# Kernel tuning notes

Hardware: AMD Instinct MI355X
Metric: run time of the kernel (lower is better)

## Reference

```python
import jax, jax.numpy as jnp
import numpy as np

B, N, H = 2, 2048, 1024
NUM_HEADS, HEAD_DIM = 16, 64
SCALE = HEAD_DIM ** -0.5


def setup_inputs() -> dict:
    key = jax.random.key(0)
    ks = jax.random.split(key, 9)
    hidden_states = jax.random.normal(ks[0], (B, N, H), dtype=jnp.float32)
    # ancestor-only mask: lower-triangular incl. diagonal (chain tree)
    tree_mask = jnp.tril(jnp.ones((N, N), dtype=jnp.int32))
    s = H ** -0.5
    Wq = jax.random.normal(ks[1], (H, NUM_HEADS * HEAD_DIM), dtype=jnp.float32) * s
    Wk = jax.random.normal(ks[2], (H, NUM_HEADS * HEAD_DIM), dtype=jnp.float32) * s
    Wv = jax.random.normal(ks[3], (H, NUM_HEADS * HEAD_DIM), dtype=jnp.float32) * s
    Wo = jax.random.normal(ks[4], (NUM_HEADS * HEAD_DIM, H), dtype=jnp.float32) * s
    bq = jnp.zeros((NUM_HEADS * HEAD_DIM,), dtype=jnp.float32)
    bk = jnp.zeros((NUM_HEADS * HEAD_DIM,), dtype=jnp.float32)
    bv = jnp.zeros((NUM_HEADS * HEAD_DIM,), dtype=jnp.float32)
    bo = jnp.zeros((H,), dtype=jnp.float32)
    return {"hidden_states": hidden_states, "tree_mask": tree_mask,
            "Wq": Wq, "bq": bq, "Wk": Wk, "bk": bk,
            "Wv": Wv, "bv": bv, "Wo": Wo, "bo": bo}


def reference(hidden_states, tree_mask, Wq, bq, Wk, bk, Wv, bv, Wo, bo):
    b, n, _ = hidden_states.shape
    q = (hidden_states @ Wq + bq).reshape(b, n, NUM_HEADS, HEAD_DIM)
    k = (hidden_states @ Wk + bk).reshape(b, n, NUM_HEADS, HEAD_DIM)
    v = (hidden_states @ Wv + bv).reshape(b, n, NUM_HEADS, HEAD_DIM)
    # scores: [b, heads, n, n]
    scores = jnp.einsum('bqhd,bkhd->bhqk', q, k) * SCALE
    neg_inf = jnp.finfo(scores.dtype).min
    scores = jnp.where(tree_mask[None, None, :, :] == 0, neg_inf, scores)
    attn = jax.nn.softmax(scores, axis=-1)  # dropout p=0.0 -> identity
    out = jnp.einsum('bhqk,bkhd->bqhd', attn, v).reshape(b, n, NUM_HEADS * HEAD_DIM)
    return out @ Wo + bo
```

## Files before the change

kernel.cpp:

```cpp
#include <hip/hip_runtime.h>
#include <hip/hip_bf16.h>
#include <stdint.h>

typedef unsigned short u16;
typedef short short8 __attribute__((ext_vector_type(8)));
typedef float f32x4 __attribute__((ext_vector_type(4)));
typedef u16 u16x4 __attribute__((ext_vector_type(4)));

#define SCLOG 0.18033688011112042f

static __device__ __forceinline__ u16 f2bf(float f) {
  unsigned u = __float_as_uint(f);
  unsigned rnd = 0x7fffu + ((u >> 16) & 1u);
  return (u16)((u + rnd) >> 16);
}

static __device__ __forceinline__ unsigned pk_bf16(float a, float b) {
  unsigned r;
  asm("v_cvt_pk_bf16_f32 %0, %1, %2" : "=v"(r) : "v"(a), "v"(b));
  return r;
}

static __device__ __forceinline__ void gload_lds16(const void* g, void* l) {
  __builtin_amdgcn_global_load_lds(
      (const __attribute__((address_space(1))) unsigned int*)g,
      (__attribute__((address_space(3))) unsigned int*)l, 16, 0, 0);
}

__global__ __launch_bounds__(256) void prep_kernel(
    const float* __restrict__ hs, const int* __restrict__ mask,
    const float* __restrict__ Wq, const float* __restrict__ Wk,
    const float* __restrict__ Wv, const float* __restrict__ Wo,
    u16* __restrict__ X, u16* __restrict__ WT,
    unsigned long long* __restrict__ bits) {
  __shared__ float tile[32][33];
  const int bid = blockIdx.x;
  const int tid = threadIdx.x;
  if (bid < 4096) {
    const int i = bid * 256 + tid;
    const float4 v = reinterpret_cast<const float4*>(hs)[i];
    u16x4 o;
    o[0] = f2bf(v.x); o[1] = f2bf(v.y); o[2] = f2bf(v.z); o[3] = f2bf(v.w);
    reinterpret_cast<u16x4*>(X)[i] = o;
  } else if (bid < 8192) {
    const int B = bid - 4096;
    const int z = B >> 10, y = (B >> 5) & 31, x = B & 31;
    const float* src = (z == 0) ? Wq : (z == 1) ? Wk : (z == 2) ? Wv : Wo;
    u16* dst = WT + (size_t)z * 1024 * 1024;
    const int row0 = y * 32, col0 = x * 32;
    const int tx = tid & 31, ty = tid >> 5;
#pragma unroll
    for (int i = 0; i < 4; ++i)
      tile[ty + i * 8][tx] = src[(size_t)(row0 + ty + i * 8) * 1024 + col0 + tx];
    __syncthreads();
#pragma unroll
    for (int i = 0; i < 4; ++i) {
      const int r = ty + i * 8;
      dst[(size_t)(col0 + r) * 1024 + row0 + tx] = f2bf(tile[tx][r]);
    }
  } else {
    const int gw = (bid - 8192) * 4 + (tid >> 6);
    const int lane = tid & 63;
    const int q = gw >> 5, w = gw & 31;
    const int mv = mask[(size_t)q * 2048 + w * 64 + lane];
    const unsigned long long bal = __ballot(mv != 0);
    if (lane == 0) bits[(size_t)q * 32 + w] = bal;
  }
}

__global__ __launch_bounds__(256) void gemm_qkv_kernel(
    const u16* __restrict__ X, const u16* __restrict__ WT,
    const float* __restrict__ bq, const float* __restrict__ bk, const float* __restrict__ bv,
    u16* __restrict__ Qb, u16* __restrict__ Kb, u16* __restrict__ Vb) {
  __shared__ u16 As[128 * 32];
  __shared__ u16 Bs[128 * 32];
  const int tid = threadIdx.x;
  const int lane = tid & 63, wid = tid >> 6;
  const int l15 = lane & 15, lg = lane >> 4;
  const int wg = blockIdx.x;
  const int xcd = wg & 7, idx = wg >> 3;
  const int n0 = (xcd * 3 + (idx >> 5)) * 128;
  const int m0 = (idx & 31) * 128;
  const int wr = wid >> 1, wc = wid & 1;

  f32x4 acc[4][4] = {};

  for (int kt = 0; kt < 32; ++kt) {
    __syncthreads();
#pragma unroll
    for (int p = 0; p < 2; ++p) {
      const int c = p * 256 + tid;
      const int r = c >> 2, ch = c & 3;
      gload_lds16(X + (size_t)(m0 + r) * 1024 + kt * 32 + ch * 8,
                  &As[(p * 256 + wid * 64) * 8]);
      gload_lds16(WT + (size_t)(n0 + r) * 1024 + kt * 32 + ch * 8,
                  &Bs[(p * 256 + wid * 64) * 8]);
    }
    __syncthreads();
    short8 af[4], bfr[4];
#pragma unroll
    for (int i = 0; i < 4; ++i) {
      af[i] = *reinterpret_cast<const short8*>(&As[(wr * 64 + i * 16 + l15) * 32 + lg * 8]);
      bfr[i] = *reinterpret_cast<const short8*>(&Bs[(wc * 64 + i * 16 + l15) * 32 + lg * 8]);
    }
#pragma unroll
    for (int i = 0; i < 4; ++i)
#pragma unroll
      for (int j = 0; j < 4; ++j)
        acc[i][j] = __builtin_amdgcn_mfma_f32_16x16x32_bf16(bfr[j], af[i], acc[i][j], 0, 0, 0);
  }

#pragma unroll
  for (int i = 0; i < 4; ++i) {
    const int m = m0 + wr * 64 + i * 16 + l15;
    const int bb = m >> 11, t = m & 2047;
#pragma unroll
    for (int j = 0; j < 4; ++j) {
      const int n = n0 + wc * 64 + j * 16 + lg * 4;
      const float* bsrc = (n < 1024) ? (bq + n) : (n < 2048) ? (bk + n - 1024) : (bv + n - 2048);
      const float4 b4 = *reinterpret_cast<const float4*>(bsrc);
      const float scl = (n < 1024) ? SCLOG : 1.0f;
      u16* dst = (n < 1024) ? Qb : (n < 2048) ? Kb : Vb;
      const int nl = n & 1023;
      const int hh = nl >> 6, d0 = nl & 63;
      uint2 pk;
      pk.x = pk_bf16((acc[i][j][0] + b4.x) * scl, (acc[i][j][1] + b4.y) * scl);
      pk.y = pk_bf16((acc[i][j][2] + b4.z) * scl, (acc[i][j][3] + b4.w) * scl);
      *reinterpret_cast<uint2*>(dst + ((size_t)(bb * 16 + hh) * 2048 + t) * 64 + d0) = pk;
    }
  }
}

__global__ __launch_bounds__(256) void transpose_v_kernel(const u16* __restrict__ Vb,
                                                          u16* __restrict__ VT) {
  __shared__ u16 tile[64][68];
  const int tid = threadIdx.x;
  const int tt = blockIdx.x & 31;
  const int bh = blockIdx.x >> 5;
  const size_t base = (size_t)bh * 2048 * 64;
  const int t0 = tt * 64;
#pragma unroll
  for (int p = 0; p < 2; ++p) {
    int i = p * 256 + tid;
    int row = i >> 3, ch = i & 7;
    *reinterpret_cast<short8*>(&tile[row][ch * 8]) =
        *reinterpret_cast<const short8*>(Vb + base + (size_t)(t0 + row) * 64 + ch * 8);
  }
  __syncthreads();
#pragma unroll
  for (int p = 0; p < 2; ++p) {
    int i = p * 256 + tid;
    int d = i >> 3, ch = i & 7;
    short8 v;
#pragma unroll
    for (int j = 0; j < 8; ++j) v[j] = tile[ch * 8 + j][d];
    *reinterpret_cast<short8*>(VT + base + (size_t)d * 2048 + t0 + ch * 8) = v;
  }
}

struct AttnState {
  f32x4 O[4];
  float l;
  short8 qf0, qf1;
};

static __device__ __forceinline__ void attn_tile(
    AttnState& st, const u16* __restrict__ Kb_, const u16* __restrict__ Vb_,
    u16* __restrict__ pwave, unsigned long long w,
    int l15, int lg, int slg) {
  f32x4 sT[4] = {};
  __builtin_amdgcn_s_setprio(1);
#pragma unroll
  for (int dc = 0; dc < 2; ++dc) {
    const short8 qv = dc ? st.qf1 : st.qf0;
#pragma unroll
    for (int sub = 0; sub < 4; ++sub) {
      const short8 kf = *reinterpret_cast<const short8*>(
          &Kb_[dc * 2048 + (sub * 16 + l15) * 32 + slg]);
      sT[sub] = __builtin_amdgcn_mfma_f32_16x16x32_bf16(kf, qv, sT[sub], 0, 0, 0);
    }
  }
  __builtin_amdgcn_s_setprio(0);

  if (!__all(w == ~0ull)) {
    const unsigned mlo = (unsigned)w, mhi = (unsigned)(w >> 32);
#pragma unroll
    for (int sub = 0; sub < 4; ++sub) {
      const unsigned f = ((sub & 2) ? mhi : mlo) >> ((sub & 1) * 16 + lg * 4);
#pragma unroll
      for (int r = 0; r < 4; ++r)
        sT[sub][r] = ((f >> r) & 1u) ? sT[sub][r] : -1e30f;
    }
  }

  float lsum = 0.f;
#pragma unroll
  for (int kc = 0; kc < 2; ++kc) {
#pragma unroll
    for (int s2 = 0; s2 < 2; ++s2) {
      const int sub = kc * 2 + s2;
      const float e0 = exp2f(sT[sub][0]);
      const float e1 = exp2f(sT[sub][1]);
      const float e2 = exp2f(sT[sub][2]);
      const float e3 = exp2f(sT[sub][3]);
      lsum += (e0 + e1) + (e2 + e3);
      uint2 pk;
      pk.x = pk_bf16(e0, e1);
      pk.y = pk_bf16(e2, e3);
      *reinterpret_cast<uint2*>(&pwave[l15 * 40 + s2 * 16 + lg * 4]) = pk;
    }
    const short8 pf = *reinterpret_cast<const short8*>(&pwave[l15 * 40 + lg * 8]);
    __builtin_amdgcn_s_setprio(1);
#pragma unroll
    for (int dt = 0; dt < 4; ++dt) {
      const short8 vf = *reinterpret_cast<const short8*>(
          &Vb_[kc * 2048 + (dt * 16 + l15) * 32 + slg]);
      st.O[dt] = __builtin_amdgcn_mfma_f32_16x16x32_bf16(vf, pf, st.O[dt], 0, 0, 0);
    }
    __builtin_amdgcn_s_setprio(0);
  }
  st.l += lsum;
}

__global__ __launch_bounds__(256, 4) void attn_kernel(
    const u16* __restrict__ Q, const u16* __restrict__ K, const u16* __restrict__ VT,
    const unsigned long long* __restrict__ MB, u16* __restrict__ AO) {
  __shared__ u16 K_lds[2][4096];
  __shared__ u16 V_lds[2][4096];
  __shared__ u16 p_lds[4][16][40];
  __shared__ unsigned actA_s, actB_s;

  const int tid = threadIdx.x;
  const int wid = tid >> 6, lane = tid & 63;
  const int l15 = lane & 15, lg = lane >> 4;

  const int wgid = blockIdx.x;
  const int x = wgid & 7, s = wgid >> 3;
  const int g = x + 8 * (s >> 5);
  const int qp = s & 31;
  const int h = g & 15, b = g >> 4;
  const int qA_t = qp, qB_t = 63 - qp;
  const size_t bh_off = ((size_t)(b * 16 + h)) * 2048 * 64;

  if (tid == 0) { actA_s = 0; actB_s = 0; }
  __syncthreads();
  {
    const int ktc = tid & 31, rg = tid >> 5;
    unsigned long long orA = 0, orB = 0;
#pragma unroll
    for (int i = 0; i < 4; ++i) {
      orA |= MB[(size_t)(qA_t * 32 + rg * 4 + i) * 32 + ktc];
      orB |= MB[(size_t)(qB_t * 32 + rg * 4 + i) * 32 + ktc];
    }
    if (orA) atomicOr(&actA_s, 1u << ktc);
    if (orB) atomicOr(&actB_s, 1u << ktc);
  }

  const int sid = wid >> 1;
  const int qt = sid ? qB_t : qA_t;
  const int q = qt * 32 + (wid & 1) * 16 + l15;

  AttnState st;
  {
    const short8* qp_ = reinterpret_cast<const short8*>(Q + bh_off + (size_t)q * 64);
    st.qf0 = qp_[lg]; st.qf1 = qp_[4 + lg];
#pragma unroll
    for (int dt = 0; dt < 4; ++dt) st.O[dt] = f32x4{};
    st.l = 0.f;
  }

  const int slg = (lg ^ ((l15 >> 1) & 3)) * 8;

  int offK[2], offV[2], ldsi[2];
#pragma unroll
  for (int p = 0; p < 2; ++p) {
    const int i = wid * 128 + p * 64 + lane;
    const int pc = i >> 8, row = (i >> 2) & 63, lgc = i & 3;
    const int lgs = lgc ^ ((i >> 3) & 3);
    offK[p] = row * 64 + pc * 32 + lgs * 8;
    offV[p] = row * 2048 + pc * 32 + lgs * 8;
    ldsi[p] = (wid * 128 + p * 64) * 8;
  }
  const u16* Kg = K + bh_off;
  const u16* Vg = VT + bh_off;
  u16* pwave = &p_lds[wid][0][0];

  __syncthreads();
  const unsigned actA = actA_s, actB = actB_s;
  const unsigned actW = sid ? actB : actA;
  unsigned rem = actA | actB;
  int buf = 0;

#define STAGE_TILE(bb, ktv)                                        \
  do {                                                             \
    const u16* ksrc_ = Kg + (ktv) * 64 * 64;                       \
    const u16* vsrc_ = Vg + (ktv) * 64;                            \
    _Pragma("unroll") for (int p_ = 0; p_ < 2; ++p_) {             \
      gload_lds16(ksrc_ + offK[p_], &K_lds[bb][ldsi[p_]]);         \
      gload_lds16(vsrc_ + offV[p_], &V_lds[bb][ldsi[p_]]);         \
    }                                                              \
  } while (0)

  if (rem) {
    int kt = __ffs(rem) - 1;
    unsigned long long w_cur = MB[(size_t)q * 32 + kt];
    STAGE_TILE(0, kt);
    __syncthreads();

    while (true) {
      rem &= rem - 1;
      int ktn = -1;
      unsigned long long w_next = 0;
      if (rem) {
        ktn = __ffs(rem) - 1;
        w_next = MB[(size_t)q * 32 + ktn];
        STAGE_TILE(buf ^ 1, ktn);
      }

      if ((actW >> kt) & 1u)
        attn_tile(st, &K_lds[buf][0], &V_lds[buf][0], pwave, w_cur, l15, lg, slg);

      if (ktn < 0) break;
      __syncthreads();
      buf ^= 1;
      kt = ktn;
      w_cur = w_next;
    }
  }
#undef STAGE_TILE

  {
    float lr = st.l;
    lr += __shfl_xor(lr, 16);
    lr += __shfl_xor(lr, 32);
    const float inv = (lr > 0.f) ? (1.0f / lr) : 0.f;
    u16* dst = AO + ((size_t)(b * 2048 + q)) * 1024 + h * 64;
#pragma unroll
    for (int dt = 0; dt < 4; ++dt) {
      uint2 pk;
      pk.x = pk_bf16(st.O[dt][0] * inv, st.O[dt][1] * inv);
      pk.y = pk_bf16(st.O[dt][2] * inv, st.O[dt][3] * inv);
      *reinterpret_cast<uint2*>(dst + dt * 16 + lg * 4) = pk;
    }
  }
}

__global__ __launch_bounds__(256) void gemm_out_kernel(
    const u16* __restrict__ A, const u16* __restrict__ BT,
    const float* __restrict__ bo, float* __restrict__ out) {
  __shared__ u16 As[128 * 32];
  __shared__ u16 Bs[128 * 32];
  const int tid = threadIdx.x;
  const int lane = tid & 63, wid = tid >> 6;
  const int l15 = lane & 15, lg = lane >> 4;
  const int wg = blockIdx.x;
  const int n0 = (wg & 7) * 128;
  const int m0 = (wg >> 3) * 128;
  const int wr = wid >> 1, wc = wid & 1;

  f32x4 acc[4][4] = {};

  for (int kt = 0; kt < 32; ++kt) {
    __syncthreads();
#pragma unroll
    for (int p = 0; p < 2; ++p) {
      const int c = p * 256 + tid;
      const int r = c >> 2, ch = c & 3;
      gload_lds16(A + (size_t)(m0 + r) * 1024 + kt * 32 + ch * 8,
                  &As[(p * 256 + wid * 64) * 8]);
      gload_lds16(BT + (size_t)(n0 + r) * 1024 + kt * 32 + ch * 8,
                  &Bs[(p * 256 + wid * 64) * 8]);
    }
    __syncthreads();
    short8 af[4], bfr[4];
#pragma unroll
    for (int i = 0; i < 4; ++i) {
      af[i] = *reinterpret_cast<const short8*>(&As[(wr * 64 + i * 16 + l15) * 32 + lg * 8]);
      bfr[i] = *reinterpret_cast<const short8*>(&Bs[(wc * 64 + i * 16 + l15) * 32 + lg * 8]);
    }
#pragma unroll
    for (int i = 0; i < 4; ++i)
#pragma unroll
      for (int j = 0; j < 4; ++j)
        acc[i][j] = __builtin_amdgcn_mfma_f32_16x16x32_bf16(bfr[j], af[i], acc[i][j], 0, 0, 0);
  }

#pragma unroll
  for (int i = 0; i < 4; ++i) {
    const int m = m0 + wr * 64 + i * 16 + l15;
#pragma unroll
    for (int j = 0; j < 4; ++j) {
      const int n = n0 + wc * 64 + j * 16 + lg * 4;
      const float4 b4 = *reinterpret_cast<const float4*>(bo + n);
      float4 o4;
      o4.x = acc[i][j][0] + b4.x;
      o4.y = acc[i][j][1] + b4.y;
      o4.z = acc[i][j][2] + b4.z;
      o4.w = acc[i][j][3] + b4.w;
      *reinterpret_cast<float4*>(out + (size_t)m * 1024 + n) = o4;
    }
  }
}

extern "C" void kernel_launch(void* const* d_in, const int* in_sizes, int n_in,
                              void* d_out, int out_size, void* d_ws, size_t ws_size,
                              hipStream_t stream) {
  (void)in_sizes; (void)n_in; (void)out_size; (void)ws_size;
  const float* hs = (const float*)d_in[0];
  const int* mask = (const int*)d_in[1];
  const float* Wq = (const float*)d_in[2];
  const float* bq = (const float*)d_in[3];
  const float* Wk = (const float*)d_in[4];
  const float* bk = (const float*)d_in[5];
  const float* Wv = (const float*)d_in[6];
  const float* bv = (const float*)d_in[7];
  const float* Wo = (const float*)d_in[8];
  const float* bo = (const float*)d_in[9];
  float* out = (float*)d_out;

  uint8_t* ws = (uint8_t*)d_ws;
  u16* X  = (u16*)(ws);
  u16* WT = (u16*)(ws + ((size_t)8 << 20));
  u16* Qb = (u16*)(ws + ((size_t)16 << 20));
  u16* Kb = (u16*)(ws + ((size_t)24 << 20));
  u16* Vb = (u16*)(ws + ((size_t)32 << 20));
  u16* AO = (u16*)(ws + ((size_t)40 << 20));
  unsigned long long* MB = (unsigned long long*)(ws + ((size_t)48 << 20));
  u16* VbT = X;

  prep_kernel<<<dim3(24576), dim3(256), 0, stream>>>(hs, mask, Wq, Wk, Wv, Wo, X, WT, MB);
  gemm_qkv_kernel<<<dim3(768), dim3(256), 0, stream>>>(X, WT, bq, bk, bv, Qb, Kb, Vb);
  transpose_v_kernel<<<dim3(1024), dim3(256), 0, stream>>>(Vb, VbT);
  attn_kernel<<<dim3(1024), dim3(256), 0, stream>>>(Qb, Kb, VbT, MB, AO);
  gemm_out_kernel<<<dim3(256), dim3(256), 0, stream>>>(AO, WT + (size_t)3072 * 1024, bo, out);
}
```

Measured before the change: 133.7 us.

## Rewrite attention with 32x32 MFMA, per-wave query tiles, and permlane P reshuffle

The attention kernel switches from 16x16x32 to 32x32x16 bf16 MFMAs, so each wave owns a full 32-query tile and four waves share one block's K/V staging. That halves the grid to 512 blocks with balanced causal pairs (p, 31-p, 32+p, 63-p). The P matrix is moved between lanes with v_permlane32_swap instead of a round trip through LDS, and the K/V LDS layout uses a new XOR swizzle. Active tiles are found with a ballot instead of shared atomics. Register pressure rises (launch bounds drop to 2 waves/SIMD) and occupancy falls, in exchange for more K/V reuse per block and fewer LDS operations.

```diff
diff --git a/kernel.cpp b/kernel.cpp
--- a/kernel.cpp
+++ b/kernel.cpp
@@ -5,9 +5,12 @@
 typedef unsigned short u16;
 typedef short short8 __attribute__((ext_vector_type(8)));
 typedef float f32x4 __attribute__((ext_vector_type(4)));
+typedef float f32x16 __attribute__((ext_vector_type(16)));
 typedef u16 u16x4 __attribute__((ext_vector_type(4)));
+typedef unsigned uint32x4 __attribute__((ext_vector_type(4)));
 
 #define SCLOG 0.18033688011112042f
+#define MFMA32(A, B, C) __builtin_amdgcn_mfma_f32_32x32x16_bf16(A, B, C, 0, 0, 0)
 
 static __device__ __forceinline__ u16 f2bf(float f) {
   unsigned u = __float_as_uint(f);
@@ -158,142 +161,127 @@
   }
 }
 
-struct AttnState {
-  f32x4 O[4];
-  float l;
-  short8 qf0, qf1;
-};
-
-static __device__ __forceinline__ void attn_tile(
-    AttnState& st, const u16* __restrict__ Kb_, const u16* __restrict__ Vb_,
-    u16* __restrict__ pwave, unsigned long long w,
-    int l15, int lg, int slg) {
-  f32x4 sT[4] = {};
+static __device__ __forceinline__ void attn_tile32(
+    f32x16& O0, f32x16& O1, float& lacc, const short8 qf[4],
+    const u16* __restrict__ Kb_, const u16* __restrict__ Vb_,
+    unsigned long long w, int l31, int hi) {
+  f32x16 s0 = {}, s1 = {};
+  const int r7 = l31 & 7;
   __builtin_amdgcn_s_setprio(1);
 #pragma unroll
-  for (int dc = 0; dc < 2; ++dc) {
-    const short8 qv = dc ? st.qf1 : st.qf0;
-#pragma unroll
-    for (int sub = 0; sub < 4; ++sub) {
-      const short8 kf = *reinterpret_cast<const short8*>(
-          &Kb_[dc * 2048 + (sub * 16 + l15) * 32 + slg]);
-      sT[sub] = __builtin_amdgcn_mfma_f32_16x16x32_bf16(kf, qv, sT[sub], 0, 0, 0);
-    }
+  for (int dc = 0; dc < 4; ++dc) {
+    const int sl = (dc * 2 + hi) ^ r7;
+    const short8 kf0 = *reinterpret_cast<const short8*>(&Kb_[l31 * 64 + sl * 8]);
+    const short8 kf1 = *reinterpret_cast<const short8*>(&Kb_[(32 + l31) * 64 + sl * 8]);
+    s0 = MFMA32(kf0, qf[dc], s0);
+    s1 = MFMA32(kf1, qf[dc], s1);
   }
   __builtin_amdgcn_s_setprio(0);
 
-  if (!__all(w == ~0ull)) {
-    const unsigned mlo = (unsigned)w, mhi = (unsigned)(w >> 32);
-#pragma unroll
-    for (int sub = 0; sub < 4; ++sub) {
-      const unsigned f = ((sub & 2) ? mhi : mlo) >> ((sub & 1) * 16 + lg * 4);
-#pragma unroll
-      for (int r = 0; r < 4; ++r)
-        sT[sub][r] = ((f >> r) & 1u) ? sT[sub][r] : -1e30f;
-    }
-  }
-
-  float lsum = 0.f;
-#pragma unroll
-  for (int kc = 0; kc < 2; ++kc) {
-#pragma unroll
-    for (int s2 = 0; s2 < 2; ++s2) {
-      const int sub = kc * 2 + s2;
-      const float e0 = exp2f(sT[sub][0]);
-      const float e1 = exp2f(sT[sub][1]);
-      const float e2 = exp2f(sT[sub][2]);
-      const float e3 = exp2f(sT[sub][3]);
-      lsum += (e0 + e1) + (e2 + e3);
-      uint2 pk;
-      pk.x = pk_bf16(e0, e1);
-      pk.y = pk_bf16(e2, e3);
-      *reinterpret_cast<uint2*>(&pwave[l15 * 40 + s2 * 16 + lg * 4]) = pk;
-    }
-    const short8 pf = *reinterpret_cast<const short8*>(&pwave[l15 * 40 + lg * 8]);
-    __builtin_amdgcn_s_setprio(1);
-#pragma unroll
-    for (int dt = 0; dt < 4; ++dt) {
-      const short8 vf = *reinterpret_cast<const short8*>(
-          &Vb_[kc * 2048 + (dt * 16 + l15) * 32 + slg]);
-      st.O[dt] = __builtin_amdgcn_mfma_f32_16x16x32_bf16(vf, pf, st.O[dt], 0, 0, 0);
-    }
-    __builtin_amdgcn_s_setprio(0);
-  }
-  st.l += lsum;
-}
-
-__global__ __launch_bounds__(256, 4) void attn_kernel(
+  const bool full = __all(w == ~0ull);
+  float ls = 0.f;
+#pragma unroll
+  for (int kc2 = 0; kc2 < 2; ++kc2) {
+    f32x16 sv = kc2 ? s1 : s0;
+    if (!full) {
+      const unsigned fk = ((unsigned)(w >> (kc2 * 32))) >> (4 * hi);
+#pragma unroll
+      for (int g = 0; g < 4; ++g)
+#pragma unroll
+        for (int e = 0; e < 4; ++e)
+          if (!((fk >> (8 * g + e)) & 1u)) sv[g * 4 + e] = -1e30f;
+    }
+    float pe[16];
+#pragma unroll
+    for (int r = 0; r < 16; ++r) { pe[r] = exp2f(sv[r]); ls += pe[r]; }
+    unsigned u0 = pk_bf16(pe[0], pe[1]),  u1 = pk_bf16(pe[2], pe[3]);
+    unsigned u2 = pk_bf16(pe[4], pe[5]),  u3 = pk_bf16(pe[6], pe[7]);
+    unsigned u4 = pk_bf16(pe[8], pe[9]),  u5 = pk_bf16(pe[10], pe[11]);
+    unsigned u6 = pk_bf16(pe[12], pe[13]), u7 = pk_bf16(pe[14], pe[15]);
+    asm volatile("v_permlane32_swap_b32 %0, %1" : "+v"(u0), "+v"(u2));
+    asm volatile("v_permlane32_swap_b32 %0, %1" : "+v"(u1), "+v"(u3));
+    asm volatile("v_permlane32_swap_b32 %0, %1" : "+v"(u4), "+v"(u6));
+    asm volatile("v_permlane32_swap_b32 %0, %1" : "+v"(u5), "+v"(u7));
+    uint32x4 f0; f0[0] = u0; f0[1] = u1; f0[2] = u2; f0[3] = u3;
+    uint32x4 f1; f1[0] = u4; f1[1] = u5; f1[2] = u6; f1[3] = u7;
+#pragma unroll
+    for (int j = 0; j < 2; ++j) {
+      const short8 pa = __builtin_bit_cast(short8, j ? f1 : f0);
+      const int kc = kc2 * 2 + j;
+      const int sl = (kc * 2 + hi) ^ r7;
+      const short8 vf0 = *reinterpret_cast<const short8*>(&Vb_[l31 * 64 + sl * 8]);
+      const short8 vf1 = *reinterpret_cast<const short8*>(&Vb_[(32 + l31) * 64 + sl * 8]);
+      __builtin_amdgcn_s_setprio(1);
+      O0 = MFMA32(vf0, pa, O0);
+      O1 = MFMA32(vf1, pa, O1);
+      __builtin_amdgcn_s_setprio(0);
+    }
+  }
+  lacc += ls;
+}
+
+__global__ __launch_bounds__(256, 2) void attn_kernel(
     const u16* __restrict__ Q, const u16* __restrict__ K, const u16* __restrict__ VT,
     const unsigned long long* __restrict__ MB, u16* __restrict__ AO) {
   __shared__ u16 K_lds[2][4096];
   __shared__ u16 V_lds[2][4096];
-  __shared__ u16 p_lds[4][16][40];
-  __shared__ unsigned actA_s, actB_s;
+  __shared__ unsigned act_s[4];
 
   const int tid = threadIdx.x;
   const int wid = tid >> 6, lane = tid & 63;
-  const int l15 = lane & 15, lg = lane >> 4;
+  const int l31 = lane & 31, hi = lane >> 5;
 
   const int wgid = blockIdx.x;
   const int x = wgid & 7, s = wgid >> 3;
-  const int g = x + 8 * (s >> 5);
-  const int qp = s & 31;
+  const int g = x + 8 * (s >> 4);
+  const int p = s & 15;
   const int h = g & 15, b = g >> 4;
-  const int qA_t = qp, qB_t = 63 - qp;
   const size_t bh_off = ((size_t)(b * 16 + h)) * 2048 * 64;
 
-  if (tid == 0) { actA_s = 0; actB_s = 0; }
-  __syncthreads();
+  const int qt = (wid == 0) ? p : (wid == 1) ? 31 - p : (wid == 2) ? 32 + p : 63 - p;
+  const int qbase = qt * 32;
+  const int q = qbase + l31;
+
   {
-    const int ktc = tid & 31, rg = tid >> 5;
-    unsigned long long orA = 0, orB = 0;
-#pragma unroll
-    for (int i = 0; i < 4; ++i) {
-      orA |= MB[(size_t)(qA_t * 32 + rg * 4 + i) * 32 + ktc];
-      orB |= MB[(size_t)(qB_t * 32 + rg * 4 + i) * 32 + ktc];
-    }
-    if (orA) atomicOr(&actA_s, 1u << ktc);
-    if (orB) atomicOr(&actB_s, 1u << ktc);
-  }
-
-  const int sid = wid >> 1;
-  const int qt = sid ? qB_t : qA_t;
-  const int q = qt * 32 + (wid & 1) * 16 + l15;
-
-  AttnState st;
+    unsigned long long orw = 0;
+#pragma unroll
+    for (int i = 0; i < 16; ++i)
+      orw |= MB[(size_t)(qbase + hi * 16 + i) * 32 + l31];
+    const unsigned long long bal = __ballot(orw != 0);
+    if (lane == 0) act_s[wid] = (unsigned)bal | (unsigned)(bal >> 32);
+  }
+
+  short8 qf[4];
   {
-    const short8* qp_ = reinterpret_cast<const short8*>(Q + bh_off + (size_t)q * 64);
-    st.qf0 = qp_[lg]; st.qf1 = qp_[4 + lg];
-#pragma unroll
-    for (int dt = 0; dt < 4; ++dt) st.O[dt] = f32x4{};
-    st.l = 0.f;
-  }
-
-  const int slg = (lg ^ ((l15 >> 1) & 3)) * 8;
+    const short8* qp8 = reinterpret_cast<const short8*>(Q + bh_off + (size_t)q * 64);
+#pragma unroll
+    for (int dc = 0; dc < 4; ++dc) qf[dc] = qp8[dc * 2 + hi];
+  }
+
+  f32x16 O0 = {}, O1 = {};
+  float lacc = 0.f;
 
   int offK[2], offV[2], ldsi[2];
 #pragma unroll
-  for (int p = 0; p < 2; ++p) {
-    const int i = wid * 128 + p * 64 + lane;
-    const int pc = i >> 8, row = (i >> 2) & 63, lgc = i & 3;
-    const int lgs = lgc ^ ((i >> 3) & 3);
-    offK[p] = row * 64 + pc * 32 + lgs * 8;
-    offV[p] = row * 2048 + pc * 32 + lgs * 8;
-    ldsi[p] = (wid * 128 + p * 64) * 8;
+  for (int pp = 0; pp < 2; ++pp) {
+    const int i = pp * 256 + tid;
+    const int row = i >> 3, cs = i & 7;
+    const int c = cs ^ (row & 7);
+    offK[pp] = row * 64 + c * 8;
+    offV[pp] = row * 2048 + c * 8;
+    ldsi[pp] = i * 8;
   }
   const u16* Kg = K + bh_off;
   const u16* Vg = VT + bh_off;
-  u16* pwave = &p_lds[wid][0][0];
 
   __syncthreads();
-  const unsigned actA = actA_s, actB = actB_s;
-  const unsigned actW = sid ? actB : actA;
-  unsigned rem = actA | actB;
+  const unsigned actW = act_s[wid];
+  unsigned rem = act_s[0] | act_s[1] | act_s[2] | act_s[3];
   int buf = 0;
 
 #define STAGE_TILE(bb, ktv)                                        \
   do {                                                             \
-    const u16* ksrc_ = Kg + (ktv) * 64 * 64;                       \
+    const u16* ksrc_ = Kg + (ktv) * 4096;                          \
     const u16* vsrc_ = Vg + (ktv) * 64;                            \
     _Pragma("unroll") for (int p_ = 0; p_ < 2; ++p_) {             \
       gload_lds16(ksrc_ + offK[p_], &K_lds[bb][ldsi[p_]]);         \
@@ -318,7 +306,7 @@
       }
 
       if ((actW >> kt) & 1u)
-        attn_tile(st, &K_lds[buf][0], &V_lds[buf][0], pwave, w_cur, l15, lg, slg);
+        attn_tile32(O0, O1, lacc, qf, &K_lds[buf][0], &V_lds[buf][0], w_cur, l31, hi);
 
       if (ktn < 0) break;
       __syncthreads();
@@ -330,17 +318,19 @@
 #undef STAGE_TILE
 
   {
-    float lr = st.l;
-    lr += __shfl_xor(lr, 16);
-    lr += __shfl_xor(lr, 32);
+    const float lr = lacc + __shfl_xor(lacc, 32);
     const float inv = (lr > 0.f) ? (1.0f / lr) : 0.f;
     u16* dst = AO + ((size_t)(b * 2048 + q)) * 1024 + h * 64;
 #pragma unroll
-    for (int dt = 0; dt < 4; ++dt) {
-      uint2 pk;
-      pk.x = pk_bf16(st.O[dt][0] * inv, st.O[dt][1] * inv);
-      pk.y = pk_bf16(st.O[dt][2] * inv, st.O[dt][3] * inv);
-      *reinterpret_cast<uint2*>(dst + dt * 16 + lg * 4) = pk;
+    for (int dt = 0; dt < 2; ++dt) {
+      const f32x16 Ov = dt ? O1 : O0;
+#pragma unroll
+      for (int gg = 0; gg < 4; ++gg) {
+        uint2 pk;
+        pk.x = pk_bf16(Ov[gg * 4 + 0] * inv, Ov[gg * 4 + 1] * inv);
+        pk.y = pk_bf16(Ov[gg * 4 + 2] * inv, Ov[gg * 4 + 3] * inv);
+        *reinterpret_cast<uint2*>(dst + dt * 32 + gg * 8 + hi * 4) = pk;
+      }
     }
   }
 }
@@ -431,6 +421,6 @@
   prep_kernel<<<dim3(24576), dim3(256), 0, stream>>>(hs, mask, Wq, Wk, Wv, Wo, X, WT, MB);
   gemm_qkv_kernel<<<dim3(768), dim3(256), 0, stream>>>(X, WT, bq, bk, bv, Qb, Kb, Vb);
   transpose_v_kernel<<<dim3(1024), dim3(256), 0, stream>>>(Vb, VbT);
-  attn_kernel<<<dim3(1024), dim3(256), 0, stream>>>(Qb, Kb, VbT, MB, AO);
+  attn_kernel<<<dim3(512), dim3(256), 0, stream>>>(Qb, Kb, VbT, MB, AO);
   gemm_out_kernel<<<dim3(256), dim3(256), 0, stream>>>(AO, WT + (size_t)3072 * 1024, bo, out);
 }
```

Result: slower. 140.2 us (+4.9%).
